# Kernel tuning notes

Measured on AMD Instinct MI355X. Metric: run time of the kernel, lower is better.

## Reference

```python
import jax, jax.numpy as jnp
import numpy as np

NF, NV = 200000, 100000
C_IN, MULT, K = 128, 2, 16
C_OUT = 128
BN_EPS = 1e-3


def setup_inputs() -> dict:
    key = jax.random.key(0)
    ks = jax.random.split(key, 8)
    inputs = jax.random.normal(ks[0], (NF, C_IN), dtype=jnp.float32)
    filt_coeff = jax.random.uniform(ks[1], (NF, K), dtype=jnp.float32)
    face = jax.random.randint(ks[2], (NF, 3), 0, NV, dtype=jnp.int32)
    nf_count = jax.random.randint(ks[3], (NV,), 0, 12, dtype=jnp.int32)
    vt_map = jnp.arange(NV, dtype=jnp.int32)
    # parameters (xavier-normal-like init for weights)
    sw_std = float(np.sqrt(2.0 / (C_IN + MULT)))
    spatial_weights = jax.random.normal(ks[4], (K, C_IN, MULT), dtype=jnp.float32) * sw_std
    dw_std = float(np.sqrt(2.0 / (C_IN * MULT + C_OUT)))
    depth_weights = jax.random.normal(ks[5], (C_IN * MULT, C_OUT), dtype=jnp.float32) * dw_std
    biases = jnp.zeros((1, C_OUT), dtype=jnp.float32)
    gamma = jnp.ones((C_OUT,), dtype=jnp.float32)
    beta = jnp.zeros((C_OUT,), dtype=jnp.float32)
    return {"inputs": inputs, "filt_coeff": filt_coeff, "face": face,
            "nf_count": nf_count, "vt_map": vt_map,
            "spatial_weights": spatial_weights, "depth_weights": depth_weights,
            "biases": biases, "gamma": gamma, "beta": beta}


def reference(inputs, filt_coeff, face, nf_count, vt_map,
              spatial_weights, depth_weights, biases, gamma, beta):
    Nf, C = inputs.shape
    Kb, _, M = spatial_weights.shape
    Nv = nf_count.shape[0]
    # per-face mixture kernel:  w[f,c,m] = sum_k filt_coeff[f,k] * spatial_weights[k,c,m]
    w = jnp.einsum('fk,kcm->fcm', filt_coeff, spatial_weights)
    feat = (inputs[:, :, None] * w).reshape(Nf, C * M)  # [Nf, C*M]
    # scatter facet features to the 3 incident vertices (mapped via vt_map)
    tgt = vt_map[face]  # [Nf, 3]
    agg = jnp.zeros((Nv, C * M), dtype=feat.dtype)
    for j in range(3):  # small fixed structural loop (3 verts per triangle)
        agg = agg + jax.ops.segment_sum(feat, tgt[:, j], num_segments=Nv)
    denom = jnp.maximum(nf_count, 1).astype(feat.dtype)[:, None]
    vert = agg / denom  # mean over incident facets, [Nv, C*M]
    # dense depthwise (pointwise) matmul + bias + ReLU
    out = vert @ depth_weights + biases
    out = jax.nn.relu(out)
    # BatchNorm1d (training-mode batch statistics, eps=1e-3)
    mean = out.mean(axis=0)
    var = out.var(axis=0)
    out = (out - mean) * jax.lax.rsqrt(var + BN_EPS) * gamma + beta
    return out
```

## Files before the change

kernel.cpp:

```cpp
#include <hip/hip_runtime.h>
#include <hip/hip_bf16.h>


constexpr int C_IN  = 128;
constexpr int KF    = 16;
constexpr int CM    = 256;
constexpr int C_OUT = 128;
constexpr int CAP   = 32;
constexpr int GB    = 1024;
constexpr int FT    = 64;
constexpr float BN_EPS = 1e-3f;

typedef __attribute__((ext_vector_type(8))) short short8;
typedef __attribute__((ext_vector_type(4))) float f32x4;

__device__ __forceinline__ ushort f2bf(float x) {
  union { float f; unsigned u; } v; v.f = x;
  return (ushort)((v.u + 0x7fffu + ((v.u >> 16) & 1u)) >> 16);
}
__device__ __forceinline__ float b2f(ushort u) {
  return __uint_as_float((unsigned)u << 16);
}
__device__ __forceinline__ uint pk2(float a, float b) {
  __hip_bfloat162 h = __float22bfloat162_rn(float2{a, b});
  return *(uint*)&h;
}
__device__ __forceinline__ void dma16(const float* g, void* l) {
  __builtin_amdgcn_global_load_lds(
      (const __attribute__((address_space(1))) void*)g,
      (__attribute__((address_space(3))) void*)l, 16, 0, 0);
}

__global__ __launch_bounds__(256) void k_prep(const float* __restrict__ dw,
                                              const float* __restrict__ sw,
                                              ushort* __restrict__ dwt,
                                              ushort* __restrict__ swt) {
  const int b = blockIdx.x, tid = threadIdx.x;
  if (b < 64) {
    int i = b * 512 + tid;
#pragma unroll
    for (int r = 0; r < 2; ++r, i += 256) {
      int n = i >> 8, k = i & 255;
      dwt[i] = f2bf(dw[k * C_OUT + n]);
    }
  } else {
    int i = (b - 64) * 256 + tid;
    int cm = i >> 5, k = i & 31;
    swt[i] = (k < KF) ? f2bf(sw[k * CM + cm]) : (ushort)0;
  }
}

__global__ __launch_bounds__(256) void k_fill(
    const int* __restrict__ face, const int* __restrict__ vt_map,
    int* __restrict__ cnt, int* __restrict__ slots, int n_inc) {
  int i = blockIdx.x * blockDim.x + threadIdx.x;
  if (i < n_inc) {
    int f = i / 3;
    int v = vt_map[face[i]];
    int p = atomicAdd(&cnt[v], 1);
    if (p < CAP) slots[(size_t)v * CAP + p] = f;
  }
}

__global__ __launch_bounds__(256, 4) void k_faceg(
    const float* __restrict__ inp, const float* __restrict__ fc,
    const ushort* __restrict__ swt, const ushort* __restrict__ dwt,
    ushort* __restrict__ g) {
  __shared__ __align__(1024) ushort s_buf[FT * 256];
  char* s_bytes = (char*)s_buf;

  const int tid  = threadIdx.x;
  const int w    = tid >> 6;
  const int lane = tid & 63;
  const int rm   = lane & 15;
  const int kg   = lane >> 4;
  const int fb   = blockIdx.x * FT;

#pragma unroll
  for (int it = 0; it < 8; ++it) {
    const int row   = w * 16 + it * 2 + (lane >> 5);
    const int chunk = lane & 31;
    const float* src = inp + (size_t)(fb + row) * C_IN + ((chunk ^ (row & 7)) << 2);
    dma16(src, s_bytes + w * 8192 + it * 1024);
  }

  short8 a1[4];
#pragma unroll
  for (int ct = 0; ct < 4; ++ct)
    a1[ct] = *(const short8*)&swt[(size_t)(w * 64 + ct * 16 + rm) * 32 + kg * 8];

  short8 b1[4];
#pragma unroll
  for (int ft = 0; ft < 4; ++ft) {
    const float* fr = &fc[(size_t)(fb + ft * 16 + rm) * KF + (kg & 1) * 8];
    const float4 p0 = *(const float4*)fr;
    const float4 p1 = *(const float4*)(fr + 4);
    uint4 u;
    u.x = pk2(p0.x, p0.y); u.y = pk2(p0.z, p0.w);
    u.z = pk2(p1.x, p1.y); u.w = pk2(p1.z, p1.w);
    if (kg >= 2) u = uint4{0, 0, 0, 0};
    b1[ft] = *(short8*)&u;
  }

  asm volatile("s_waitcnt vmcnt(0)" ::: "memory");
  __syncthreads();

#pragma unroll
  for (int ft = 0; ft < 4; ++ft) {
#pragma unroll
    for (int ct = 0; ct < 4; ++ct) {
      f32x4 acc = {0.f, 0.f, 0.f, 0.f};
      acc = __builtin_amdgcn_mfma_f32_16x16x32_bf16(a1[ct], b1[ft], acc, 0, 0, 0);
      const int face = ft * 16 + rm;
      const int cmb  = w * 64 + ct * 16 + kg * 4;
      const int byt  = face * 512 + ((((cmb * 2) >> 4) ^ (face & 7)) << 4)
                     + ((cmb * 2) & 15);
      const float2 ivv = *(const float2*)(s_bytes + byt);
      uint2 pw;
      pw.x = pk2(acc[0] * ivv.x, acc[1] * ivv.x);
      pw.y = pk2(acc[2] * ivv.y, acc[3] * ivv.y);
      *(uint2*)(s_bytes + byt) = pw;
    }
  }

  short8 bfr[2][8];
#pragma unroll
  for (int nt = 0; nt < 2; ++nt) {
    const int n = (w * 2 + nt) * 16 + rm;
#pragma unroll
    for (int ks = 0; ks < 8; ++ks)
      bfr[nt][ks] = *(const short8*)&dwt[n * 256 + ks * 32 + kg * 8];
  }
  __syncthreads();

  f32x4 acc2[4][2];
#pragma unroll
  for (int fs = 0; fs < 4; ++fs)
#pragma unroll
    for (int nt = 0; nt < 2; ++nt)
      acc2[fs][nt] = (f32x4){0.f, 0.f, 0.f, 0.f};

#pragma unroll
  for (int fs = 0; fs < 4; ++fs)
#pragma unroll
    for (int ks = 0; ks < 8; ++ks) {
      const int row = fs * 16 + rm;
      const int byt = row * 512 + (((ks * 4 + kg) ^ (row & 7)) << 4);
      const short8 af = *(const short8*)(s_bytes + byt);
      acc2[fs][0] = __builtin_amdgcn_mfma_f32_16x16x32_bf16(af, bfr[0][ks], acc2[fs][0], 0, 0, 0);
      acc2[fs][1] = __builtin_amdgcn_mfma_f32_16x16x32_bf16(af, bfr[1][ks], acc2[fs][1], 0, 0, 0);
    }
  __syncthreads();

#pragma unroll
  for (int fs = 0; fs < 4; ++fs)
#pragma unroll
    for (int nt = 0; nt < 2; ++nt)
#pragma unroll
      for (int r = 0; r < 4; ++r) {
        const int row = fs * 16 + kg * 4 + r;
        const int col = (w * 2 + nt) * 16 + rm;
        const int byt = row * 512 + (((col >> 2) ^ (row & 7)) << 4) + (col & 3) * 4;
        *(float*)(s_bytes + byt) = acc2[fs][nt][r];
      }
  __syncthreads();

  const int irow = tid >> 2;
  const int cb   = (tid & 3) * 32;
#pragma unroll
  for (int i = 0; i < 4; ++i) {
    const int c0 = (cb + 8 * i) >> 2;
    const float4 a = *(const float4*)(s_bytes + irow * 512 + ((c0 ^ (irow & 7)) << 4));
    const float4 b = *(const float4*)(s_bytes + irow * 512 + (((c0 + 1) ^ (irow & 7)) << 4));
    uint4 u;
    u.x = pk2(a.x, a.y); u.y = pk2(a.z, a.w);
    u.z = pk2(b.x, b.y); u.w = pk2(b.z, b.w);
    *(short8*)&g[(size_t)(fb + irow) * C_OUT + cb + 8 * i] = *(short8*)&u;
  }
}

__global__ __launch_bounds__(256) void k_gather(
    const ushort* __restrict__ g, const int* __restrict__ cnt,
    const int* __restrict__ slots, const int* __restrict__ nf_cnt,
    const float* __restrict__ bias, float* __restrict__ out,
    float* __restrict__ part, int nv, int ntiles) {
  __shared__ float s_red[256][8];

  const int tid = threadIdx.x;
  const int q   = tid & 15;
  const int vg  = tid >> 4;
  const int c8  = q * 8;

  float bs[8];
#pragma unroll
  for (int j = 0; j < 8; ++j) bs[j] = bias[c8 + j];
  float st_s[8], st_q[8];
#pragma unroll
  for (int j = 0; j < 8; ++j) { st_s[j] = 0.f; st_q[j] = 0.f; }

  for (int tile = blockIdx.x; tile < ntiles; tile += gridDim.x) {
    const int v = tile * 16 + vg;
    int deg = cnt[v]; deg = deg > CAP ? CAP : deg;
    const int* sl = &slots[(size_t)v * CAP];

    float a[8];
#pragma unroll
    for (int j = 0; j < 8; ++j) a[j] = 0.f;

    int t = 0;
    for (; t + 4 <= deg; t += 4) {
      const int4 ff = *(const int4*)&sl[t];
      const short8 r0 = *(const short8*)&g[(size_t)ff.x * C_OUT + c8];
      const short8 r1 = *(const short8*)&g[(size_t)ff.y * C_OUT + c8];
      const short8 r2 = *(const short8*)&g[(size_t)ff.z * C_OUT + c8];
      const short8 r3 = *(const short8*)&g[(size_t)ff.w * C_OUT + c8];
#pragma unroll
      for (int j = 0; j < 8; ++j)
        a[j] += (b2f((ushort)r0[j]) + b2f((ushort)r1[j]))
              + (b2f((ushort)r2[j]) + b2f((ushort)r3[j]));
    }
    for (; t < deg; ++t) {
      const short8 r0 = *(const short8*)&g[(size_t)sl[t] * C_OUT + c8];
#pragma unroll
      for (int j = 0; j < 8; ++j) a[j] += b2f((ushort)r0[j]);
    }

    int d = nf_cnt[v]; if (d < 1) d = 1;
    const float inv = 1.0f / (float)d;
    float r[8];
#pragma unroll
    for (int j = 0; j < 8; ++j) {
      r[j] = fmaxf(fmaf(a[j], inv, bs[j]), 0.f);
      st_s[j] += r[j];
      st_q[j] = fmaf(r[j], r[j], st_q[j]);
    }
    *(float4*)&out[(size_t)v * C_OUT + c8]     = make_float4(r[0], r[1], r[2], r[3]);
    *(float4*)&out[(size_t)v * C_OUT + c8 + 4] = make_float4(r[4], r[5], r[6], r[7]);
  }

#pragma unroll
  for (int j = 0; j < 8; ++j) s_red[tid][j] = st_s[j];
  __syncthreads();
  if (tid < 16) {
    for (int j = 0; j < 8; ++j) {
      float x = 0.f;
      for (int gg = 0; gg < 16; ++gg) x += s_red[gg * 16 + tid][j];
      part[(size_t)(tid * 8 + j) * GB + blockIdx.x] = x;
    }
  }
  __syncthreads();
#pragma unroll
  for (int j = 0; j < 8; ++j) s_red[tid][j] = st_q[j];
  __syncthreads();
  if (tid < 16) {
    for (int j = 0; j < 8; ++j) {
      float x = 0.f;
      for (int gg = 0; gg < 16; ++gg) x += s_red[gg * 16 + tid][j];
      part[(size_t)(128 + tid * 8 + j) * GB + blockIdx.x] = x;
    }
  }
}

__global__ __launch_bounds__(256) void k_red(const float* __restrict__ part,
                                             float* __restrict__ red) {
  const int j   = blockIdx.x;
  const int tid = threadIdx.x;
  float v = 0.f;
#pragma unroll
  for (int b = 0; b < GB; b += 256) v += part[(size_t)j * GB + b + tid];
#pragma unroll
  for (int off = 32; off > 0; off >>= 1) v += __shfl_down(v, off);
  __shared__ float sred[4];
  if ((tid & 63) == 0) sred[tid >> 6] = v;
  __syncthreads();
  if (tid == 0) red[j] = sred[0] + sred[1] + sred[2] + sred[3];
}

__global__ void k_fin(const float* __restrict__ red,
                      const float* __restrict__ gamma, const float* __restrict__ beta,
                      float* __restrict__ scale, float* __restrict__ shift, float invN) {
  int o = threadIdx.x;
  float mean = red[o] * invN;
  float var  = red[128 + o] * invN - mean * mean;
  float sc   = gamma[o] * rsqrtf(var + BN_EPS);
  scale[o] = sc;
  shift[o] = fmaf(-mean, sc, beta[o]);
}

__global__ __launch_bounds__(256) void k_bn(float* __restrict__ out,
                                            const float* __restrict__ scale,
                                            const float* __restrict__ shift, int n4) {
  int idx = blockIdx.x * blockDim.x + threadIdx.x;
  int stride = gridDim.x * blockDim.x;
  for (; idx < n4; idx += stride) {
    float4 v = ((const float4*)out)[idx];
    int base = (idx * 4) & (C_OUT - 1);
    float4 sc = *(const float4*)&scale[base];
    float4 sh = *(const float4*)&shift[base];
    v.x = fmaf(v.x, sc.x, sh.x);
    v.y = fmaf(v.y, sc.y, sh.y);
    v.z = fmaf(v.z, sc.z, sh.z);
    v.w = fmaf(v.w, sc.w, sh.w);
    ((float4*)out)[idx] = v;
  }
}

extern "C" void kernel_launch(void* const* d_in, const int* in_sizes, int n_in,
                              void* d_out, int out_size, void* d_ws, size_t ws_size,
                              hipStream_t stream) {
  const float* inputs = (const float*)d_in[0];
  const float* fc     = (const float*)d_in[1];
  const int*   face   = (const int*)d_in[2];
  const int*   nf_cnt = (const int*)d_in[3];
  const int*   vt_map = (const int*)d_in[4];
  const float* sw     = (const float*)d_in[5];
  const float* dw     = (const float*)d_in[6];
  const float* bias   = (const float*)d_in[7];
  const float* gamma  = (const float*)d_in[8];
  const float* beta   = (const float*)d_in[9];
  float* out = (float*)d_out;

  const int nf = in_sizes[0] / C_IN;
  const int nv = in_sizes[3];

  char* p = (char*)d_ws;
  int*    cnt   = (int*)p;            p += (size_t)nv * 4;
  float*  scale = (float*)p;          p += C_OUT * 4;
  float*  shift = (float*)p;          p += C_OUT * 4;
  float*  red   = (float*)p;          p += 256 * 4;
  float*  part  = (float*)p;          p += (size_t)256 * GB * 4;
  ushort* dwt   = (ushort*)p;         p += (size_t)C_OUT * CM * 2;
  ushort* swt   = (ushort*)p;         p += (size_t)CM * 32 * 2;
  int*    slots = (int*)p;            p += (size_t)nv * CAP * 4;
  ushort* g     = (ushort*)p;

  hipMemsetAsync(cnt, 0, (size_t)nv * 4, stream);

  k_prep<<<96, 256, 0, stream>>>(dw, sw, dwt, swt);

  const int n_inc = nf * 3;
  k_fill<<<(n_inc + 255) / 256, 256, 0, stream>>>(face, vt_map, cnt, slots, n_inc);

  const int ntiles_f = (nf + FT - 1) / FT;
  k_faceg<<<ntiles_f, 256, 0, stream>>>(inputs, fc, swt, dwt, g);

  const int ntiles_v = (nv + 15) / 16;
  k_gather<<<GB, 256, 0, stream>>>(g, cnt, slots, nf_cnt, bias, out, part, nv, ntiles_v);

  k_red<<<256, 256, 0, stream>>>(part, red);
  k_fin<<<1, 128, 0, stream>>>(red, gamma, beta, scale, shift, 1.0f / (float)nv);

  const int n4 = (nv * C_OUT) / 4;
  k_bn<<<4096, 256, 0, stream>>>(out, scale, shift, n4);
}
```

Before: 159.5 us.

## Make face kernel persistent with double-buffered LDS input prefetch

Turns k_faceg into a persistent kernel over a fixed grid of 512 blocks. Each block loops over face tiles, issuing the async global-to-LDS DMA for the next tile into a second buffer while it computes the current one. This is meant to hide input-load latency and amortise the per-block loads of the weight fragments. In exchange, LDS per block doubles, occupancy drops to 2 blocks per CU, and the output store column mapping is rearranged.

```diff
diff --git a/kernel.cpp b/kernel.cpp
--- a/kernel.cpp
+++ b/kernel.cpp
@@ -9,6 +9,7 @@
 constexpr int CAP   = 32;
 constexpr int GB    = 1024;
 constexpr int FT    = 64;
+constexpr int GRIDF = 512;
 constexpr float BN_EPS = 1e-3f;
 
 typedef __attribute__((ext_vector_type(8))) short short8;
@@ -29,6 +30,15 @@
   __builtin_amdgcn_global_load_lds(
       (const __attribute__((address_space(1))) void*)g,
       (__attribute__((address_space(3))) void*)l, 16, 0, 0);
+}
+__device__ __forceinline__ void bar_raw() {
+  __builtin_amdgcn_s_barrier();
+  asm volatile("" ::: "memory");
+}
+__device__ __forceinline__ void bar_lds() {
+  asm volatile("s_waitcnt lgkmcnt(0)" ::: "memory");
+  __builtin_amdgcn_s_barrier();
+  asm volatile("" ::: "memory");
 }
 
 __global__ __launch_bounds__(256) void k_prep(const float* __restrict__ dw,
@@ -62,67 +72,22 @@
   }
 }
 
-__global__ __launch_bounds__(256, 4) void k_faceg(
+__global__ __launch_bounds__(256, 2) void k_faceg(
     const float* __restrict__ inp, const float* __restrict__ fc,
     const ushort* __restrict__ swt, const ushort* __restrict__ dwt,
-    ushort* __restrict__ g) {
-  __shared__ __align__(1024) ushort s_buf[FT * 256];
-  char* s_bytes = (char*)s_buf;
+    ushort* __restrict__ g, int ntiles) {
+  __shared__ __align__(1024) ushort s_buf[2][FT * 256];
 
   const int tid  = threadIdx.x;
   const int w    = tid >> 6;
   const int lane = tid & 63;
   const int rm   = lane & 15;
   const int kg   = lane >> 4;
-  const int fb   = blockIdx.x * FT;
-
-#pragma unroll
-  for (int it = 0; it < 8; ++it) {
-    const int row   = w * 16 + it * 2 + (lane >> 5);
-    const int chunk = lane & 31;
-    const float* src = inp + (size_t)(fb + row) * C_IN + ((chunk ^ (row & 7)) << 2);
-    dma16(src, s_bytes + w * 8192 + it * 1024);
-  }
 
   short8 a1[4];
 #pragma unroll
   for (int ct = 0; ct < 4; ++ct)
     a1[ct] = *(const short8*)&swt[(size_t)(w * 64 + ct * 16 + rm) * 32 + kg * 8];
-
-  short8 b1[4];
-#pragma unroll
-  for (int ft = 0; ft < 4; ++ft) {
-    const float* fr = &fc[(size_t)(fb + ft * 16 + rm) * KF + (kg & 1) * 8];
-    const float4 p0 = *(const float4*)fr;
-    const float4 p1 = *(const float4*)(fr + 4);
-    uint4 u;
-    u.x = pk2(p0.x, p0.y); u.y = pk2(p0.z, p0.w);
-    u.z = pk2(p1.x, p1.y); u.w = pk2(p1.z, p1.w);
-    if (kg >= 2) u = uint4{0, 0, 0, 0};
-    b1[ft] = *(short8*)&u;
-  }
-
-  asm volatile("s_waitcnt vmcnt(0)" ::: "memory");
-  __syncthreads();
-
-#pragma unroll
-  for (int ft = 0; ft < 4; ++ft) {
-#pragma unroll
-    for (int ct = 0; ct < 4; ++ct) {
-      f32x4 acc = {0.f, 0.f, 0.f, 0.f};
-      acc = __builtin_amdgcn_mfma_f32_16x16x32_bf16(a1[ct], b1[ft], acc, 0, 0, 0);
-      const int face = ft * 16 + rm;
-      const int cmb  = w * 64 + ct * 16 + kg * 4;
-      const int byt  = face * 512 + ((((cmb * 2) >> 4) ^ (face & 7)) << 4)
-                     + ((cmb * 2) & 15);
-      const float2 ivv = *(const float2*)(s_bytes + byt);
-      uint2 pw;
-      pw.x = pk2(acc[0] * ivv.x, acc[1] * ivv.x);
-      pw.y = pk2(acc[2] * ivv.y, acc[3] * ivv.y);
-      *(uint2*)(s_bytes + byt) = pw;
-    }
-  }
-
   short8 bfr[2][8];
 #pragma unroll
   for (int nt = 0; nt < 2; ++nt) {
@@ -131,51 +96,121 @@
     for (int ks = 0; ks < 8; ++ks)
       bfr[nt][ks] = *(const short8*)&dwt[n * 256 + ks * 32 + kg * 8];
   }
-  __syncthreads();
-
-  f32x4 acc2[4][2];
-#pragma unroll
-  for (int fs = 0; fs < 4; ++fs)
-#pragma unroll
-    for (int nt = 0; nt < 2; ++nt)
-      acc2[fs][nt] = (f32x4){0.f, 0.f, 0.f, 0.f};
-
-#pragma unroll
-  for (int fs = 0; fs < 4; ++fs)
-#pragma unroll
-    for (int ks = 0; ks < 8; ++ks) {
-      const int row = fs * 16 + rm;
-      const int byt = row * 512 + (((ks * 4 + kg) ^ (row & 7)) << 4);
-      const short8 af = *(const short8*)(s_bytes + byt);
-      acc2[fs][0] = __builtin_amdgcn_mfma_f32_16x16x32_bf16(af, bfr[0][ks], acc2[fs][0], 0, 0, 0);
-      acc2[fs][1] = __builtin_amdgcn_mfma_f32_16x16x32_bf16(af, bfr[1][ks], acc2[fs][1], 0, 0, 0);
-    }
-  __syncthreads();
-
-#pragma unroll
-  for (int fs = 0; fs < 4; ++fs)
-#pragma unroll
-    for (int nt = 0; nt < 2; ++nt)
-#pragma unroll
-      for (int r = 0; r < 4; ++r) {
-        const int row = fs * 16 + kg * 4 + r;
-        const int col = (w * 2 + nt) * 16 + rm;
-        const int byt = row * 512 + (((col >> 2) ^ (row & 7)) << 4) + (col & 3) * 4;
-        *(float*)(s_bytes + byt) = acc2[fs][nt][r];
+
+  auto issue_dma = [&](int buf, int fb) {
+#pragma unroll
+    for (int it = 0; it < 8; ++it) {
+      const int row   = w * 16 + it * 2 + (lane >> 5);
+      const int chunk = lane & 31;
+      const float* src = inp + (size_t)(fb + row) * C_IN + ((chunk ^ (row & 7)) << 2);
+      dma16(src, (char*)s_buf + buf * 32768 + w * 8192 + it * 1024);
+    }
+  };
+
+  int t = blockIdx.x;
+  issue_dma(0, t * FT);
+  int cur = 0;
+
+  for (; t < ntiles; t += GRIDF, cur ^= 1) {
+    const int fb = t * FT;
+    char* sb = (char*)s_buf + cur * 32768;
+
+    bar_lds();
+
+    float4 p0[4], p1[4];
+#pragma unroll
+    for (int ft = 0; ft < 4; ++ft) {
+      const float* fr = &fc[(size_t)(fb + ft * 16 + rm) * KF + (kg & 1) * 8];
+      p0[ft] = *(const float4*)fr;
+      p1[ft] = *(const float4*)(fr + 4);
+    }
+
+    const int tn = t + GRIDF;
+    if (tn < ntiles) {
+      issue_dma(cur ^ 1, tn * FT);
+      asm volatile("s_waitcnt vmcnt(8)" ::: "memory");
+    } else {
+      asm volatile("s_waitcnt vmcnt(0)" ::: "memory");
+    }
+
+    short8 b1[4];
+#pragma unroll
+    for (int ft = 0; ft < 4; ++ft) {
+      uint4 u;
+      u.x = pk2(p0[ft].x, p0[ft].y); u.y = pk2(p0[ft].z, p0[ft].w);
+      u.z = pk2(p1[ft].x, p1[ft].y); u.w = pk2(p1[ft].z, p1[ft].w);
+      if (kg >= 2) u = uint4{0, 0, 0, 0};
+      b1[ft] = *(short8*)&u;
+    }
+
+    bar_raw();
+
+#pragma unroll
+    for (int ft = 0; ft < 4; ++ft) {
+#pragma unroll
+      for (int ct = 0; ct < 4; ++ct) {
+        f32x4 acc = {0.f, 0.f, 0.f, 0.f};
+        acc = __builtin_amdgcn_mfma_f32_16x16x32_bf16(a1[ct], b1[ft], acc, 0, 0, 0);
+        const int face = ft * 16 + rm;
+        const int cmb  = w * 64 + ct * 16 + kg * 4;
+        const int byt  = face * 512 + ((((cmb * 2) >> 4) ^ (face & 7)) << 4)
+                       + ((cmb * 2) & 15);
+        const float2 ivv = *(const float2*)(sb + byt);
+        uint2 pw;
+        pw.x = pk2(acc[0] * ivv.x, acc[1] * ivv.x);
+        pw.y = pk2(acc[2] * ivv.y, acc[3] * ivv.y);
+        *(uint2*)(sb + byt) = pw;
       }
-  __syncthreads();
-
-  const int irow = tid >> 2;
-  const int cb   = (tid & 3) * 32;
-#pragma unroll
-  for (int i = 0; i < 4; ++i) {
-    const int c0 = (cb + 8 * i) >> 2;
-    const float4 a = *(const float4*)(s_bytes + irow * 512 + ((c0 ^ (irow & 7)) << 4));
-    const float4 b = *(const float4*)(s_bytes + irow * 512 + (((c0 + 1) ^ (irow & 7)) << 4));
-    uint4 u;
-    u.x = pk2(a.x, a.y); u.y = pk2(a.z, a.w);
-    u.z = pk2(b.x, b.y); u.w = pk2(b.z, b.w);
-    *(short8*)&g[(size_t)(fb + irow) * C_OUT + cb + 8 * i] = *(short8*)&u;
+    }
+
+    bar_lds();
+
+    f32x4 acc2[4][2];
+#pragma unroll
+    for (int fs = 0; fs < 4; ++fs)
+#pragma unroll
+      for (int nt = 0; nt < 2; ++nt)
+        acc2[fs][nt] = (f32x4){0.f, 0.f, 0.f, 0.f};
+
+#pragma unroll
+    for (int fs = 0; fs < 4; ++fs)
+#pragma unroll
+      for (int ks = 0; ks < 8; ++ks) {
+        const int row = fs * 16 + rm;
+        const int byt = row * 512 + (((ks * 4 + kg) ^ (row & 7)) << 4);
+        const short8 af = *(const short8*)(sb + byt);
+        acc2[fs][0] = __builtin_amdgcn_mfma_f32_16x16x32_bf16(af, bfr[0][ks], acc2[fs][0], 0, 0, 0);
+        acc2[fs][1] = __builtin_amdgcn_mfma_f32_16x16x32_bf16(af, bfr[1][ks], acc2[fs][1], 0, 0, 0);
+      }
+
+    bar_lds();
+
+#pragma unroll
+    for (int fs = 0; fs < 4; ++fs)
+#pragma unroll
+      for (int nt = 0; nt < 2; ++nt)
+#pragma unroll
+        for (int r = 0; r < 4; ++r) {
+          const int row = fs * 16 + kg * 4 + r;
+          const int col = (w * 2 + nt) * 16 + rm;
+          const int byt = row * 512 + (((col >> 2) ^ (row & 7)) << 4) + (col & 3) * 4;
+          *(float*)(sb + byt) = acc2[fs][nt][r];
+        }
+
+    bar_lds();
+
+    const int irow = tid >> 2;
+    const int q    = tid & 3;
+#pragma unroll
+    for (int i = 0; i < 4; ++i) {
+      const int c0 = 2 * q + 8 * i;
+      const float4 a = *(const float4*)(sb + irow * 512 + ((c0 ^ (irow & 7)) << 4));
+      const float4 b = *(const float4*)(sb + irow * 512 + (((c0 + 1) ^ (irow & 7)) << 4));
+      uint4 u;
+      u.x = pk2(a.x, a.y); u.y = pk2(a.z, a.w);
+      u.z = pk2(b.x, b.y); u.w = pk2(b.z, b.w);
+      *(short8*)&g[(size_t)(fb + irow) * C_OUT + c0 * 4] = *(short8*)&u;
+    }
   }
 }
 
@@ -342,7 +377,7 @@
   k_fill<<<(n_inc + 255) / 256, 256, 0, stream>>>(face, vt_map, cnt, slots, n_inc);
 
   const int ntiles_f = (nf + FT - 1) / FT;
-  k_faceg<<<ntiles_f, 256, 0, stream>>>(inputs, fc, swt, dwt, g);
+  k_faceg<<<GRIDF, 256, 0, stream>>>(inputs, fc, swt, dwt, g, ntiles_f);
 
   const int ntiles_v = (nv + 15) / 16;
   k_gather<<<GB, 256, 0, stream>>>(g, cnt, slots, nf_cnt, bias, out, part, nv, ntiles_v);
```

New measurement: 150.4 us. 1.06x faster.
